# Kernel tuning notes

Measured on AMD Instinct MI355X. Metric: run time of the kernel, lower is better.

Reference implementation:

```python
import jax, jax.numpy as jnp
import numpy as np
from jax import lax

N_SAMPLES = 2 ** 15   # 32768
N_ATOMS = 2048
ATOM_SIZE = 1024
K_SPARSE = 64
BATCH = 4


def setup_inputs() -> dict:
    key = jax.random.key(0)
    k1, k2 = jax.random.split(key)
    orig = jax.random.normal(k1, (BATCH, 1, N_SAMPLES), dtype=jnp.float32)
    # atoms ~ uniform(-1, 1) as in the torch Parameter init
    atoms = jax.random.uniform(k2, (N_ATOMS, ATOM_SIZE), dtype=jnp.float32,
                               minval=-1.0, maxval=1.0)
    return {"orig": orig, "atoms": atoms}


def reference(orig, atoms):
    B = orig.shape[0]
    # Correlate input with the atom dictionary (F.conv1d, padding=atom_size//2).
    x = lax.conv_general_dilated(
        orig, atoms.reshape(N_ATOMS, 1, ATOM_SIZE),
        window_strides=(1,), padding=[(ATOM_SIZE // 2, ATOM_SIZE // 2)],
        dimension_numbers=("NCH", "OIH", "NCH"))  # [B, n_atoms, N+1]
    x = x[..., :N_SAMPLES]                          # [B, n_atoms, N]
    # dropout(p=0.05) omitted (eval-mode / deterministic reference)

    # sparsify: per-batch top-k over the flattened (atom, time) grid
    flat = x.reshape(B, N_ATOMS * N_SAMPLES)
    values, indices = lax.top_k(flat, K_SPARSE)      # [B, K]
    atom_idx = indices // N_SAMPLES                  # [B, K]
    time_idx = indices % N_SAMPLES                   # [B, K]

    # Overlap-add synthesis: gather atom, scale, scatter-add into 2N buffer.
    contrib = atoms[atom_idx] * values[..., None]    # [B, K, atom_size]
    pos = time_idx[..., None] + jnp.arange(ATOM_SIZE)  # [B, K, atom_size]
    b_idx = jnp.arange(B)[:, None, None]
    out = jnp.zeros((B, 2 * N_SAMPLES), dtype=orig.dtype)
    out = out.at[b_idx, pos].add(contrib)
    return out[:, None, :N_SAMPLES]                  # [B, 1, N]
```

## Files before the change

### kernel.cpp

```cpp
#include <hip/hip_runtime.h>

#define NS     32768
#define NA     2048
#define ASZ    1024
#define NB     4
#define SIGC   34848
#define BM     128
#define BN     128
#define BK     128
#define TILES  4096
#define CAP    8192
#define MINT   5080
#define SSCALE 20.0f
#define BSTR   1152
#define BSZ    18432

typedef signed char s8;
typedef __attribute__((ext_vector_type(4))) int i32x4;

__device__ __forceinline__ int imax(int a, int b) { return a > b ? a : b; }

__global__ void prep_k(const float* __restrict__ atoms, const float* __restrict__ orig,
                       s8* __restrict__ abf, s8* __restrict__ sigsh,
                       float* __restrict__ sigf, int* __restrict__ wlc) {
  if (blockIdx.x == 0 && threadIdx.x == 0) *wlc = 0;
  if (blockIdx.x < NA) {
    int a = blockIdx.x;
    const float* srow = atoms + (size_t)a * ASZ;
    s8* drow = abf + (size_t)a * ASZ;
    for (int k = threadIdx.x; k < ASZ; k += 256) {
      float q = fminf(127.f, fmaxf(-127.f, srow[k] * 127.f));
      drow[k] = (s8)__float2int_rn(q);
    }
  } else {
    int r = blockIdx.x - NA;
    int nch = (SIGC + 255) / 256;
    int bm = r / nch, chunk = r % nch;
    int i = chunk * 256 + threadIdx.x;
    if (i >= SIGC) return;
    int b = bm >> 4, m = bm & 15;
    int j = i + m - 512;
    float f = (j >= 0 && j < NS) ? orig[(size_t)b * NS + j] : 0.0f;
    float q = fminf(127.f, fmaxf(-127.f, f * SSCALE));
    sigsh[(size_t)bm * SIGC + i] = (s8)__float2int_rn(q);
    if (m == 0) sigf[(size_t)b * SIGC + i] = f;
  }
}

__device__ __forceinline__ void stage_bsig(const s8* __restrict__ Sb, int t0,
                                           s8* Bsig, int w, int lane) {
  #pragma unroll
  for (int i = 0; i < 5; i++) {
    int c = w + 4 * i;
    if (c < 18) {
      int o = c * 1024 + lane * 16;
      int m = o / BSTR;
      int pp = (o - m * BSTR) >> 4;
      int s = (pp & ~7) | ((pp ^ m) & 7);
      const s8* src = Sb + (size_t)m * SIGC + t0 + (s << 4);
      __builtin_amdgcn_global_load_lds((const __attribute__((address_space(1))) void*)src,
          (__attribute__((address_space(3))) void*)(&Bsig[c * 1024]), 16, 0, 0);
    }
  }
}

__device__ __forceinline__ void stage_a(const s8* __restrict__ Ab, int k0,
                                        s8* Al, int w, int lane) {
  int lr = lane >> 3, ls = lane & 7, cs = ls ^ lr;
  #pragma unroll
  for (int i = 0; i < 4; i++) {
    int c = w * 4 + i;
    const s8* src = Ab + (size_t)(c * 8 + lr) * ASZ + k0 + cs * 16;
    __builtin_amdgcn_global_load_lds((const __attribute__((address_space(1))) void*)src,
        (__attribute__((address_space(3))) void*)(&Al[c * 1024]), 16, 0, 0);
  }
}

__device__ __forceinline__ void compute_tile(const s8* Al, const s8* Bsig, int kt,
                                             int w, int lane, i32x4 acc[4][4]) {
  int wr = w >> 1, wc = w & 1;
  int arow0 = wr * 64 + (lane & 15);
  int kgrp = lane >> 4;
  int m = lane & 15, mx = m & 7;
  const s8* brow = Bsig + m * BSTR;
  int sb = wc * 4 + kgrp;
  #pragma unroll
  for (int kk = 0; kk < 2; kk++) {
    int sl = kk * 4 + kgrp;
    i32x4 af[4], bfr[4];
    #pragma unroll
    for (int mf = 0; mf < 4; mf++)
      af[mf] = *(const i32x4*)&Al[arow0 * BK + mf * 2048 + ((sl ^ (arow0 & 7)) << 4)];
    #pragma unroll
    for (int nf = 0; nf < 4; nf++) {
      int s = sb + nf + kk * 4 + kt * 8;
      int ps = (s & ~7) | ((s ^ mx) & 7);
      bfr[nf] = *(const i32x4*)&brow[ps << 4];
    }
    __builtin_amdgcn_s_setprio(1);
    #pragma unroll
    for (int mf = 0; mf < 4; mf++)
      #pragma unroll
      for (int nf = 0; nf < 4; nf++)
        acc[mf][nf] = __builtin_amdgcn_mfma_i32_16x16x64_i8(af[mf], bfr[nf], acc[mf][nf], 0, 0, 0);
    __builtin_amdgcn_s_setprio(0);
  }
}

#define K_LOOP(Ab, Sb, t0)                                    \
  stage_bsig(Sb, t0, Bsig, w, lane);                          \
  for (int kt = 0; kt < 8; kt++) {                            \
    stage_a(Ab, kt * BK, Al, w, lane);                        \
    __syncthreads();                                          \
    compute_tile(Al, Bsig, kt, w, lane, acc);                 \
    __syncthreads();                                          \
  }

__global__ __launch_bounds__(256, 4)
void screen1(const s8* __restrict__ abf, const s8* __restrict__ sigsh,
             int* __restrict__ tmax)
{
  __shared__ __align__(16) s8 Al[BM * BK];
  __shared__ __align__(16) s8 Bsig[BSZ];
  __shared__ int wred[4];
  int bid0 = blockIdx.x;
  int bid  = (bid0 & 7) * ((NB * TILES) >> 3) + (bid0 >> 3);
  int b = bid >> 12, tile = bid & 4095;
  int mt = tile >> 8, nt = tile & 255;
  int m0 = mt * BM, t0 = nt * BN;
  int tid = threadIdx.x, w = tid >> 6, lane = tid & 63;
  const s8* Ab = abf + (size_t)m0 * ASZ;
  const s8* Sb = sigsh + (size_t)b * 16 * SIGC;

  i32x4 acc[4][4];
  #pragma unroll
  for (int i = 0; i < 4; i++)
    #pragma unroll
    for (int j = 0; j < 4; j++) acc[i][j] = (i32x4){0, 0, 0, 0};

  K_LOOP(Ab, Sb, t0)

  int lmax = -2147483647;
  #pragma unroll
  for (int mf = 0; mf < 4; mf++)
    #pragma unroll
    for (int nf = 0; nf < 4; nf++)
      #pragma unroll
      for (int q = 0; q < 4; q++) lmax = imax(lmax, acc[mf][nf][q]);
  #pragma unroll
  for (int off = 32; off; off >>= 1) lmax = imax(lmax, __shfl_xor(lmax, off, 64));
  if (lane == 0) wred[w] = lmax;
  __syncthreads();
  if (tid == 0)
    tmax[b * TILES + tile] = imax(imax(wred[0], wred[1]), imax(wred[2], wred[3]));
}

__global__ void thresh_k(const int* __restrict__ tmax, int* __restrict__ thr,
                         int* __restrict__ ccnt, int* __restrict__ wl, int* __restrict__ wlc) {
  int b = blockIdx.x, tid = threadIdx.x;
  __shared__ int hist[4096];
  __shared__ int tsum[256];
  __shared__ int hist2[256];
  __shared__ int sB1, sAbove, sThr;
  for (int i = tid; i < 4096; i += 256) hist[i] = 0;
  __syncthreads();
  for (int i = tid; i < TILES; i += 256) {
    unsigned u = (unsigned)tmax[b * TILES + i] ^ 0x80000000u;
    atomicAdd(&hist[u >> 20], 1);
  }
  __syncthreads();
  { int s = 0;
    for (int j = 0; j < 16; j++) s += hist[tid * 16 + j];
    tsum[tid] = s; }
  __syncthreads();
  if (tid == 0) {
    int cum = 0, T = 0;
    for (int t2 = 255; t2 >= 0; t2--) {
      if (cum + tsum[t2] >= 64) { T = t2; break; }
      cum += tsum[t2];
    }
    int B1 = T * 16;
    for (int bk = T * 16 + 15; bk >= T * 16; bk--) {
      if (cum + hist[bk] >= 64) { B1 = bk; break; }
      cum += hist[bk];
    }
    sB1 = B1; sAbove = cum;
  }
  __syncthreads();
  if (tid < 256) hist2[tid] = 0;
  __syncthreads();
  int B1 = sB1;
  for (int i = tid; i < TILES; i += 256) {
    unsigned u = (unsigned)tmax[b * TILES + i] ^ 0x80000000u;
    if ((int)(u >> 20) == B1) atomicAdd(&hist2[(u >> 12) & 255], 1);
  }
  __syncthreads();
  if (tid == 0) {
    int cum = sAbove, B2 = 0;
    for (int z = 255; z >= 0; z--) { cum += hist2[z]; if (cum >= 64) { B2 = z; break; } }
    unsigned ulow = ((unsigned)B1 << 20) | ((unsigned)B2 << 12);
    int t = (int)(ulow ^ 0x80000000u);
    sThr = t; thr[b] = t; ccnt[b] = 0;
  }
  __syncthreads();
  int cut = sThr - MINT;
  for (int i = tid; i < TILES; i += 256)
    if (tmax[b * TILES + i] >= cut) { int p = atomicAdd(wlc, 1); wl[p] = (b << 12) | i; }
}

__global__ __launch_bounds__(256, 4)
void screen2(const s8* __restrict__ abf, const s8* __restrict__ sigsh,
             const int* __restrict__ thr, const int* __restrict__ wl,
             const int* __restrict__ wlc, int* __restrict__ ccnt, int* __restrict__ cidx)
{
  __shared__ __align__(16) s8 Al[BM * BK];
  __shared__ __align__(16) s8 Bsig[BSZ];
  int n = *wlc; if (n > NB * TILES) n = NB * TILES;
  int tid = threadIdx.x, w = tid >> 6, lane = tid & 63;
  int wr = w >> 1, wc = w & 1;
  int kgrp = lane >> 4;

  for (int wi = blockIdx.x; wi < n; wi += gridDim.x) {
    int e = wl[wi];
    int b = e >> 12, tile = e & 4095;
    int cut = thr[b] - MINT;
    int mt = tile >> 8, nt = tile & 255;
    int m0 = mt * BM, t0 = nt * BN;
    const s8* Ab = abf + (size_t)m0 * ASZ;
    const s8* Sb = sigsh + (size_t)b * 16 * SIGC;

    i32x4 acc[4][4];
    #pragma unroll
    for (int i = 0; i < 4; i++)
      #pragma unroll
      for (int j = 0; j < 4; j++) acc[i][j] = (i32x4){0, 0, 0, 0};

    K_LOOP(Ab, Sb, t0)

    int rb = m0 + wr * 64 + 4 * kgrp;
    int cb = t0 + wc * 64 + (lane & 15);
    #pragma unroll
    for (int mf = 0; mf < 4; mf++)
      #pragma unroll
      for (int nf = 0; nf < 4; nf++)
        #pragma unroll
        for (int q = 0; q < 4; q++) {
          if (acc[mf][nf][q] >= cut) {
            int a = rb + mf * 16 + q;
            int t = cb + nf * 16;
            int p = atomicAdd(&ccnt[b], 1);
            if (p < CAP) cidx[b * CAP + p] = (a << 15) | t;
          }
        }
    __syncthreads();
  }
}

__global__ void rescore_k(const float* __restrict__ atoms, const float* __restrict__ sigf,
                          const int* __restrict__ ccnt, const int* __restrict__ cidx,
                          float* __restrict__ cval) {
  int nwv = gridDim.x * 4;
  int gw = blockIdx.x * 4 + (threadIdx.x >> 6);
  int lane = threadIdx.x & 63;
  for (int b = 0; b < NB; b++) {
    int cnt = ccnt[b]; if (cnt > CAP) cnt = CAP;
    for (int ci = gw; ci < cnt; ci += nwv) {
      int idx = cidx[b * CAP + ci];
      int a = idx >> 15, t = idx & (NS - 1);
      const float* ap = atoms + (size_t)a * ASZ;
      const float* sp = sigf + (size_t)b * SIGC + t;
      float sum = 0.f;
      #pragma unroll
      for (int j = 0; j < 16; j++) { int k = lane + 64 * j; sum += ap[k] * sp[k]; }
      #pragma unroll
      for (int off = 32; off; off >>= 1) sum += __shfl_xor(sum, off, 64);
      if (lane == 0) cval[b * CAP + ci] = sum;
    }
  }
}

__global__ void select_k(const int* __restrict__ ccnt, const float* __restrict__ cval,
                         const int* __restrict__ cidx, float* __restrict__ sval,
                         int* __restrict__ sidx) {
  int b = blockIdx.x, tid = threadIdx.x;
  int cnt = ccnt[b]; if (cnt > CAP) cnt = CAP;
  __shared__ float lv[2048];
  __shared__ int li[2048];
  for (int ii = 0; ii * 256 < cnt; ii++) {
    int i = ii * 256 + tid;
    float vi = 0.f; int idi = 0; bool act = i < cnt;
    if (act) { vi = cval[b * CAP + i]; idi = cidx[b * CAP + i]; }
    int rank = 0;
    for (int c0 = 0; c0 < cnt; c0 += 2048) {
      int mchunk = cnt - c0; if (mchunk > 2048) mchunk = 2048;
      __syncthreads();
      for (int j = tid; j < mchunk; j += 256) {
        lv[j] = cval[b * CAP + c0 + j];
        li[j] = cidx[b * CAP + c0 + j];
      }
      __syncthreads();
      if (act)
        for (int j = 0; j < mchunk; j++)
          rank += (lv[j] > vi) || (lv[j] == vi && li[j] < idi);
    }
    if (act && rank < 64) { sval[b * 64 + rank] = vi; sidx[b * 64 + rank] = idi; }
  }
}

__global__ void recon_k(const float* __restrict__ atoms, const float* __restrict__ sval,
                        const int* __restrict__ sidx, float* __restrict__ out) {
  int gp = blockIdx.x * 256 + threadIdx.x;
  int b = gp >> 15, p = gp & (NS - 1);
  __shared__ float vv[64];
  __shared__ int ii[64];
  if (threadIdx.x < 64) {
    vv[threadIdx.x] = sval[b * 64 + threadIdx.x];
    ii[threadIdx.x] = sidx[b * 64 + threadIdx.x];
  }
  __syncthreads();
  float acc = 0.f;
  for (int s = 0; s < 64; s++) {
    int idx = ii[s];
    int a = idx >> 15, t = idx & (NS - 1);
    int off = p - t;
    if (off >= 0 && off < ASZ) acc += vv[s] * atoms[(size_t)a * ASZ + off];
  }
  out[gp] = acc;
}

extern "C" void kernel_launch(void* const* d_in, const int* in_sizes, int n_in,
                              void* d_out, int out_size, void* d_ws, size_t ws_size,
                              hipStream_t stream) {
  const float* orig  = (const float*)d_in[0];
  const float* atoms = (const float*)d_in[1];
  float* out = (float*)d_out;
  char* ws = (char*)d_ws;

  s8*    abf   = (s8*)   (ws + 0);
  s8*    sigsh = (s8*)   (ws + 2097152);
  float* sigf  = (float*)(ws + 4327424);
  int*   tmax  = (int*)  (ws + 4884992);
  int*   thr   = (int*)  (ws + 4950528);
  int*   ccnt  = (int*)  (ws + 4950784);
  float* cval  = (float*)(ws + 4951040);
  int*   cidx  = (int*)  (ws + 5082112);
  float* sval  = (float*)(ws + 5213184);
  int*   sidx  = (int*)  (ws + 5214208);
  int*   wl    = (int*)  (ws + 5215232);
  int*   wlc   = (int*)  (ws + 5280768);

  int nch = (SIGC + 255) / 256;
  prep_k<<<NA + NB * 16 * nch, 256, 0, stream>>>(atoms, orig, abf, sigsh, sigf, wlc);
  screen1<<<NB * TILES, 256, 0, stream>>>(abf, sigsh, tmax);
  thresh_k<<<NB, 256, 0, stream>>>(tmax, thr, ccnt, wl, wlc);
  screen2<<<512, 256, 0, stream>>>(abf, sigsh, thr, wl, wlc, ccnt, cidx);
  rescore_k<<<128, 256, 0, stream>>>(atoms, sigf, ccnt, cidx, cval);
  select_k<<<NB, 256, 0, stream>>>(ccnt, cval, cidx, sval, sidx);
  recon_k<<<out_size / 256, 256, 0, stream>>>(atoms, sval, sidx, out);
}
```

Before: 313.4 us.

## Load atom A-fragments directly from global memory instead of staging through LDS

Removes the LDS staging of the atom (A) tile and the two barriers per k-step. Each wave now reads its MFMA A operands straight from global memory (relying on L2/L1 caching), while the signal tile stays in LDS. The k-loop is unrolled by two and launch bounds drop to 3 blocks/SM to leave room for more registers. The trade is less LDS and synchronisation against uncoalesced 16-byte global loads with higher latency and possibly lower occupancy.

```diff
diff --git a/kernel.cpp b/kernel.cpp
--- a/kernel.cpp
+++ b/kernel.cpp
@@ -64,36 +64,25 @@
   }
 }
 
-__device__ __forceinline__ void stage_a(const s8* __restrict__ Ab, int k0,
-                                        s8* Al, int w, int lane) {
-  int lr = lane >> 3, ls = lane & 7, cs = ls ^ lr;
-  #pragma unroll
-  for (int i = 0; i < 4; i++) {
-    int c = w * 4 + i;
-    const s8* src = Ab + (size_t)(c * 8 + lr) * ASZ + k0 + cs * 16;
-    __builtin_amdgcn_global_load_lds((const __attribute__((address_space(1))) void*)src,
-        (__attribute__((address_space(3))) void*)(&Al[c * 1024]), 16, 0, 0);
-  }
-}
-
-__device__ __forceinline__ void compute_tile(const s8* Al, const s8* Bsig, int kt,
+__device__ __forceinline__ void compute_tile(const s8* __restrict__ Ab, const s8* Bsig, int kt,
                                              int w, int lane, i32x4 acc[4][4]) {
   int wr = w >> 1, wc = w & 1;
   int arow0 = wr * 64 + (lane & 15);
   int kgrp = lane >> 4;
   int m = lane & 15, mx = m & 7;
   const s8* brow = Bsig + m * BSTR;
-  int sb = wc * 4 + kgrp;
+  const s8* abase = Ab + (size_t)arow0 * ASZ + kt * BK;
+  int sb = wc * 4 + kgrp + kt * 8;
   #pragma unroll
   for (int kk = 0; kk < 2; kk++) {
     int sl = kk * 4 + kgrp;
     i32x4 af[4], bfr[4];
     #pragma unroll
     for (int mf = 0; mf < 4; mf++)
-      af[mf] = *(const i32x4*)&Al[arow0 * BK + mf * 2048 + ((sl ^ (arow0 & 7)) << 4)];
+      af[mf] = *(const i32x4*)&abase[(size_t)mf * 16 * ASZ + (sl << 4)];
     #pragma unroll
     for (int nf = 0; nf < 4; nf++) {
-      int s = sb + nf + kk * 4 + kt * 8;
+      int s = sb + nf + kk * 4;
       int ps = (s & ~7) | ((s ^ mx) & 7);
       bfr[nf] = *(const i32x4*)&brow[ps << 4];
     }
@@ -109,18 +98,15 @@
 
 #define K_LOOP(Ab, Sb, t0)                                    \
   stage_bsig(Sb, t0, Bsig, w, lane);                          \
-  for (int kt = 0; kt < 8; kt++) {                            \
-    stage_a(Ab, kt * BK, Al, w, lane);                        \
-    __syncthreads();                                          \
-    compute_tile(Al, Bsig, kt, w, lane, acc);                 \
-    __syncthreads();                                          \
-  }
-
-__global__ __launch_bounds__(256, 4)
+  __syncthreads();                                            \
+  _Pragma("unroll 2")                                         \
+  for (int kt = 0; kt < 8; kt++)                              \
+    compute_tile(Ab, Bsig, kt, w, lane, acc);
+
+__global__ __launch_bounds__(256, 3)
 void screen1(const s8* __restrict__ abf, const s8* __restrict__ sigsh,
              int* __restrict__ tmax)
 {
-  __shared__ __align__(16) s8 Al[BM * BK];
   __shared__ __align__(16) s8 Bsig[BSZ];
   __shared__ int wred[4];
   int bid0 = blockIdx.x;
@@ -208,12 +194,11 @@
     if (tmax[b * TILES + i] >= cut) { int p = atomicAdd(wlc, 1); wl[p] = (b << 12) | i; }
 }
 
-__global__ __launch_bounds__(256, 4)
+__global__ __launch_bounds__(256, 3)
 void screen2(const s8* __restrict__ abf, const s8* __restrict__ sigsh,
              const int* __restrict__ thr, const int* __restrict__ wl,
              const int* __restrict__ wlc, int* __restrict__ ccnt, int* __restrict__ cidx)
 {
-  __shared__ __align__(16) s8 Al[BM * BK];
   __shared__ __align__(16) s8 Bsig[BSZ];
   int n = *wlc; if (n > NB * TILES) n = NB * TILES;
   int tid = threadIdx.x, w = tid >> 6, lane = tid & 63;
```

Result: slower. 553.3 us (+76.6%).
